# Kernel tuning notes

Measured on AMD Instinct MI355X. Metric: run time of the kernel, lower is better.

The kernel has to match this reference:

```python
import jax, jax.numpy as jnp
import numpy as np
from jax import lax

N_TRACES = 128
TRACE_LEN = 32          # uniform trace length -> seq_len
INPUT_DIM = 64
HIDDEN_DIM = 128
BATCH = N_TRACES * TRACE_LEN  # 4096 events = batch_size


def setup_inputs() -> dict:
    key = jax.random.key(0)
    ks = jax.random.split(key, 12)
    s = 1.0 / np.sqrt(HIDDEN_DIM)
    u = lambda k, shape: jax.random.uniform(k, shape, jnp.float32, -s, s)
    return {
        "input": jax.random.normal(ks[0], (BATCH, INPUT_DIM), jnp.float32),
        # layer 0 LSTM params (gate order i,f,g,o as in torch)
        "W_ih0": u(ks[1], (4 * HIDDEN_DIM, INPUT_DIM)),
        "W_hh0": u(ks[2], (4 * HIDDEN_DIM, HIDDEN_DIM)),
        "b_ih0": u(ks[3], (4 * HIDDEN_DIM,)),
        "b_hh0": u(ks[4], (4 * HIDDEN_DIM,)),
        # layer 1 LSTM params
        "W_ih1": u(ks[5], (4 * HIDDEN_DIM, HIDDEN_DIM)),
        "W_hh1": u(ks[6], (4 * HIDDEN_DIM, HIDDEN_DIM)),
        "b_ih1": u(ks[7], (4 * HIDDEN_DIM,)),
        "b_hh1": u(ks[8], (4 * HIDDEN_DIM,)),
        # final linear: hidden -> 1
        "W_lin": u(ks[9], (1, HIDDEN_DIM)),
        "b_lin": u(ks[10], (1,)),
    }


def _lstm_layer(xs, W_ih, W_hh, b_ih, b_hh):
    # xs: [T, B, D_in] time-major. Returns hidden stream [T, B, H].
    H = W_hh.shape[1]
    B = xs.shape[1]
    # precompute input projection for all timesteps
    x_proj = jnp.einsum('tbd,gd->tbg', xs, W_ih) + b_ih + b_hh  # [T,B,4H]

    def step(carry, xp):
        h, c = carry
        gates = xp + h @ W_hh.T                # [B,4H]
        i, f, g, o = jnp.split(gates, 4, axis=-1)
        i = jax.nn.sigmoid(i)
        f = jax.nn.sigmoid(f)
        g = jnp.tanh(g)
        o = jax.nn.sigmoid(o)
        c = f * c + i * g
        h = o * jnp.tanh(c)
        return (h, c), h

    h0 = jnp.zeros((B, H), xs.dtype)
    _, hs = lax.scan(step, (h0, h0), x_proj)
    return hs


def _forward(input, W_ih0, W_hh0, b_ih0, b_hh0, W_ih1, W_hh1, b_ih1, b_hh1, W_lin, b_lin):
    L, D = TRACE_LEN, INPUT_DIM
    # Prefix scatter: event k of a trace gets the padded prefix events[0..k].
    x_tr = input.reshape(N_TRACES, L, D)                       # [Ntr, L, D]
    causal = (jnp.arange(L)[None, :] <= jnp.arange(L)[:, None])  # [k, j] mask j<=k
    padded = x_tr[:, None, :, :] * causal[None, :, :, None].astype(input.dtype)  # [Ntr,L(k),L(j),D]
    padded = padded.reshape(BATCH, L, D)                       # batch-first padded sequences

    xs = jnp.transpose(padded, (1, 0, 2))                      # [L, B, D] time-major
    h1 = _lstm_layer(xs, W_ih0, W_hh0, b_ih0, b_hh0)           # [L, B, H]
    h2 = _lstm_layer(h1, W_ih1, W_hh1, b_ih1, b_hh1)           # [L, B, H]

    out = jnp.einsum('tbh,oh->tbo', h2, W_lin) + b_lin         # [L, B, 1]
    # last valid timestep gather: lengths[i]-1 = (i mod L)
    lens_m1 = jnp.tile(jnp.arange(L), N_TRACES)                # [B]
    y_pred = out[lens_m1, jnp.arange(BATCH), 0]                # [B]
    return y_pred


def reference(input, W_ih0, W_hh0, b_ih0, b_hh0, W_ih1, W_hh1, b_ih1, b_hh1, W_lin, b_lin):
    return _forward(input, W_ih0, W_hh0, b_ih0, b_hh0, W_ih1, W_hh1, b_ih1, b_hh1, W_lin, b_lin)
```

## Files before the change

kernel.cpp:

```cpp
#include <hip/hip_runtime.h>

#define N_TRACES 128
#define TLEN 32
#define IN_DIM 64
#define HID 128
#define G4 (4 * HID)
#define BATCH (N_TRACES * TLEN)


__device__ __forceinline__ float fast_sigmoid(float x) {
    return 1.0f / (1.0f + __expf(-x));
}
__device__ __forceinline__ float fast_tanh(float x) {
    return 1.0f - 2.0f / (__expf(2.0f * x) + 1.0f);
}
__device__ __forceinline__ float quad_reduce(float x) {
    x += __int_as_float(__builtin_amdgcn_update_dpp(
        0, __float_as_int(x), 0xB1 , 0xF, 0xF, true));
    x += __int_as_float(__builtin_amdgcn_update_dpp(
        0, __float_as_int(x), 0x4E , 0xF, 0xF, true));
    return x;
}

__device__ __forceinline__ void load_w(const float* __restrict__ W, int u, int s,
                                       float (&w)[4][32]) {
    #pragma unroll
    for (int i = 0; i < 4; ++i) {
        const float* wr = W + (size_t)(u + 128 * i) * HID + 32 * s;
        #pragma unroll
        for (int j = 0; j < 8; ++j) {
            float4 v = *(const float4*)(wr + 4 * j);
            w[i][4 * j + 0] = v.x; w[i][4 * j + 1] = v.y;
            w[i][4 * j + 2] = v.z; w[i][4 * j + 3] = v.w;
        }
    }
    #pragma unroll
    for (int i = 0; i < 4; ++i)
        #pragma unroll
        for (int j = 0; j < 32; ++j)
            asm volatile("" : "+v"(w[i][j]));
}

__device__ __forceinline__ void matvec_acc(const float (&w)[4][32],
                                           const float* hb, float (&acc)[4]) {
    #pragma unroll
    for (int j = 0; j < 8; ++j) {
        float4 v = *(const float4*)(hb + 4 * j);
        float hx[4] = {v.x, v.y, v.z, v.w};
        #pragma unroll
        for (int e = 0; e < 4; ++e) {
            #pragma unroll
            for (int i = 0; i < 4; ++i)
                acc[i] = fmaf(w[i][4 * j + e], hx[e], acc[i]);
        }
    }
}


template <int K>
__global__ __launch_bounds__(256) void gemm_bt(
    const float* __restrict__ A,
    const float* __restrict__ W,
    const float* __restrict__ b1,
    const float* __restrict__ b2,
    float* __restrict__ out,
    int Nld)
{
    constexpr int LD = 68;
    __shared__ float At[K][LD];
    __shared__ float Wt[K][LD];

    const int tid = threadIdx.x;
    const int m0 = blockIdx.x * 64;
    const int n0 = blockIdx.y * 64;

    const int rot = tid & 3;
    #pragma unroll
    for (int j = 0; j < K / 16; ++j) {
        const int e = 4 * (tid + 256 * j);
        const int row = e / K;
        const int k = e % K;
        float4 va = *(const float4*)(A + (size_t)(m0 + row) * K + k);
        float4 vw = *(const float4*)(W + (size_t)(n0 + row) * K + k);
        float fa[4] = {va.x, va.y, va.z, va.w};
        float fw[4] = {vw.x, vw.y, vw.z, vw.w};
        #pragma unroll
        for (int ii = 0; ii < 4; ++ii) {
            const int i = (ii + rot) & 3;
            At[k + i][row] = fa[i];
            Wt[k + i][row] = fw[i];
        }
    }
    __syncthreads();

    const int tx = tid & 15;
    const int ty = tid >> 4;
    float acc[4][4] = {};

    #pragma unroll 4
    for (int k = 0; k < K; ++k) {
        float4 a = *(const float4*)&At[k][ty * 4];
        float4 w = *(const float4*)&Wt[k][tx * 4];
        acc[0][0] = fmaf(a.x, w.x, acc[0][0]); acc[0][1] = fmaf(a.x, w.y, acc[0][1]);
        acc[0][2] = fmaf(a.x, w.z, acc[0][2]); acc[0][3] = fmaf(a.x, w.w, acc[0][3]);
        acc[1][0] = fmaf(a.y, w.x, acc[1][0]); acc[1][1] = fmaf(a.y, w.y, acc[1][1]);
        acc[1][2] = fmaf(a.y, w.z, acc[1][2]); acc[1][3] = fmaf(a.y, w.w, acc[1][3]);
        acc[2][0] = fmaf(a.z, w.x, acc[2][0]); acc[2][1] = fmaf(a.z, w.y, acc[2][1]);
        acc[2][2] = fmaf(a.z, w.z, acc[2][2]); acc[2][3] = fmaf(a.z, w.w, acc[2][3]);
        acc[3][0] = fmaf(a.w, w.x, acc[3][0]); acc[3][1] = fmaf(a.w, w.y, acc[3][1]);
        acc[3][2] = fmaf(a.w, w.z, acc[3][2]); acc[3][3] = fmaf(a.w, w.w, acc[3][3]);
    }

    float bb[4];
    #pragma unroll
    for (int j = 0; j < 4; ++j) {
        const int n = n0 + tx * 4 + j;
        bb[j] = b1[n] + b2[n];
    }
    #pragma unroll
    for (int i = 0; i < 4; ++i) {
        const int m = m0 + ty * 4 + i;
        float4 v;
        v.x = acc[i][0] + bb[0]; v.y = acc[i][1] + bb[1];
        v.z = acc[i][2] + bb[2]; v.w = acc[i][3] + bb[3];
        *(float4*)(out + (size_t)m * Nld + n0 + tx * 4) = v;
    }
}


__global__ __launch_bounds__(512) void fused_trace(
    const float* __restrict__ xproj0,
    const float* __restrict__ Whh0,
    const float* __restrict__ Wih1,
    const float* __restrict__ bih1,
    const float* __restrict__ bhh1,
    const float* __restrict__ Whh1,
    const float* __restrict__ Wlin,
    const float* __restrict__ blin,
    float* __restrict__ y)
{
    const int trace = blockIdx.x;
    const int tid = threadIdx.x;
    const int u = tid >> 2;
    const int s = tid & 3;
    const int pu = u + 4 * (u >> 5);

    __shared__ float hs[TLEN][140];
    __shared__ float xp[TLEN * G4];

    float w[4][32];

    const float* xpb = xproj0 + (size_t)trace * TLEN * G4;
    #pragma unroll
    for (int j = 0; j < 8; ++j) {
        const int f4 = j * 512 + tid;
        float4 v = *(const float4*)(xpb + 4 * f4);
        *(float4*)(&xp[4 * f4]) = v;
    }
    load_w(Whh0, u, s, w);
    __syncthreads();

    float c = 0.0f;
    #pragma unroll 1
    for (int t = 0; t < TLEN; ++t) {
        float xg[4];
        #pragma unroll
        for (int i = 0; i < 4; ++i) xg[i] = xp[t * G4 + 128 * i + u];

        float acc[4] = {0.f, 0.f, 0.f, 0.f};
        if (t > 0) matvec_acc(w, &hs[t - 1][36 * s], acc);
        #pragma unroll
        for (int i = 0; i < 4; ++i) acc[i] = quad_reduce(acc[i]);

        if (s == 0) {
            const float iv = fast_sigmoid(acc[0] + xg[0]);
            const float fv = fast_sigmoid(acc[1] + xg[1]);
            const float gv = fast_tanh(acc[2] + xg[2]);
            const float ov = fast_sigmoid(acc[3] + xg[3]);
            c = fv * c + iv * gv;
            hs[t][pu] = ov * fast_tanh(c);
        }
        __syncthreads();
    }

    load_w(Wih1, u, s, w);
    float bi[4] = {0.f, 0.f, 0.f, 0.f};
    if (s == 0) {
        #pragma unroll
        for (int i = 0; i < 4; ++i) bi[i] = bih1[u + 128 * i] + bhh1[u + 128 * i];
    }
    #pragma unroll 1
    for (int t = 0; t < TLEN; ++t) {
        float acc[4] = {0.f, 0.f, 0.f, 0.f};
        matvec_acc(w, &hs[t][36 * s], acc);
        #pragma unroll
        for (int i = 0; i < 4; ++i) acc[i] = quad_reduce(acc[i]);
        if (s == 0) {
            #pragma unroll
            for (int i = 0; i < 4; ++i) xp[t * G4 + 128 * i + u] = acc[i] + bi[i];
        }
    }
    __syncthreads();

    load_w(Whh1, u, s, w);
    c = 0.0f;
    #pragma unroll 1
    for (int t = 0; t < TLEN; ++t) {
        float xg[4];
        #pragma unroll
        for (int i = 0; i < 4; ++i) xg[i] = xp[t * G4 + 128 * i + u];

        float acc[4] = {0.f, 0.f, 0.f, 0.f};
        if (t > 0) matvec_acc(w, &hs[t - 1][36 * s], acc);
        #pragma unroll
        for (int i = 0; i < 4; ++i) acc[i] = quad_reduce(acc[i]);

        if (s == 0) {
            const float iv = fast_sigmoid(acc[0] + xg[0]);
            const float fv = fast_sigmoid(acc[1] + xg[1]);
            const float gv = fast_tanh(acc[2] + xg[2]);
            const float ov = fast_sigmoid(acc[3] + xg[3]);
            c = fv * c + iv * gv;
            hs[t][pu] = ov * fast_tanh(c);
        }
        __syncthreads();
    }

    if (tid < 128) {
        const int tq = tid >> 2;
        const int sq = tid & 3;
        float wl[32];
        #pragma unroll
        for (int j = 0; j < 8; ++j) {
            float4 v = *(const float4*)(Wlin + 32 * sq + 4 * j);
            wl[4 * j + 0] = v.x; wl[4 * j + 1] = v.y;
            wl[4 * j + 2] = v.z; wl[4 * j + 3] = v.w;
        }
        const float* hb = &hs[tq][36 * sq];
        float a = 0.f;
        #pragma unroll
        for (int j = 0; j < 8; ++j) {
            float4 v = *(const float4*)(hb + 4 * j);
            a = fmaf(v.x, wl[4 * j + 0], a);
            a = fmaf(v.y, wl[4 * j + 1], a);
            a = fmaf(v.z, wl[4 * j + 2], a);
            a = fmaf(v.w, wl[4 * j + 3], a);
        }
        a = quad_reduce(a);
        if (sq == 0) y[trace * TLEN + tq] = a + blin[0];
    }
}


extern "C" void kernel_launch(void* const* d_in, const int* in_sizes, int n_in,
                              void* d_out, int out_size, void* d_ws, size_t ws_size,
                              hipStream_t stream) {
    const float* input = (const float*)d_in[0];
    const float* W_ih0 = (const float*)d_in[1];
    const float* W_hh0 = (const float*)d_in[2];
    const float* b_ih0 = (const float*)d_in[3];
    const float* b_hh0 = (const float*)d_in[4];
    const float* W_ih1 = (const float*)d_in[5];
    const float* W_hh1 = (const float*)d_in[6];
    const float* b_ih1 = (const float*)d_in[7];
    const float* b_hh1 = (const float*)d_in[8];
    const float* W_lin = (const float*)d_in[9];
    const float* b_lin = (const float*)d_in[10];
    float* out = (float*)d_out;

    float* xproj0 = (float*)d_ws;

    dim3 ggrid(BATCH / 64, G4 / 64);

    gemm_bt<IN_DIM><<<ggrid, 256, 0, stream>>>(input, W_ih0, b_ih0, b_hh0, xproj0, G4);
    fused_trace<<<N_TRACES, 512, 0, stream>>>(xproj0, W_hh0, W_ih1, b_ih1, b_hh1,
                                              W_hh1, W_lin, b_lin, out);
}
```

Measured before the change: 167.9 us.

## Batch 16 traces per workgroup and run LSTM recurrences on bf16x3 MFMA

```diff
diff --git a/kernel.cpp b/kernel.cpp
--- a/kernel.cpp
+++ b/kernel.cpp
@@ -4,9 +4,13 @@
 #define TLEN 32
 #define IN_DIM 64
 #define HID 128
-#define G4 (4 * HID)
-#define BATCH (N_TRACES * TLEN)
-
+#define G4 512
+#define BATCH 4096
+#define WGT 16
+#define NWG 8
+
+typedef __attribute__((ext_vector_type(8))) short bf16x8;
+typedef __attribute__((ext_vector_type(4))) float f32x4;
 
 __device__ __forceinline__ float fast_sigmoid(float x) {
     return 1.0f / (1.0f + __expf(-x));
@@ -14,46 +18,12 @@
 __device__ __forceinline__ float fast_tanh(float x) {
     return 1.0f - 2.0f / (__expf(2.0f * x) + 1.0f);
 }
-__device__ __forceinline__ float quad_reduce(float x) {
-    x += __int_as_float(__builtin_amdgcn_update_dpp(
-        0, __float_as_int(x), 0xB1 , 0xF, 0xF, true));
-    x += __int_as_float(__builtin_amdgcn_update_dpp(
-        0, __float_as_int(x), 0x4E , 0xF, 0xF, true));
-    return x;
-}
-
-__device__ __forceinline__ void load_w(const float* __restrict__ W, int u, int s,
-                                       float (&w)[4][32]) {
-    #pragma unroll
-    for (int i = 0; i < 4; ++i) {
-        const float* wr = W + (size_t)(u + 128 * i) * HID + 32 * s;
-        #pragma unroll
-        for (int j = 0; j < 8; ++j) {
-            float4 v = *(const float4*)(wr + 4 * j);
-            w[i][4 * j + 0] = v.x; w[i][4 * j + 1] = v.y;
-            w[i][4 * j + 2] = v.z; w[i][4 * j + 3] = v.w;
-        }
-    }
-    #pragma unroll
-    for (int i = 0; i < 4; ++i)
-        #pragma unroll
-        for (int j = 0; j < 32; ++j)
-            asm volatile("" : "+v"(w[i][j]));
-}
-
-__device__ __forceinline__ void matvec_acc(const float (&w)[4][32],
-                                           const float* hb, float (&acc)[4]) {
-    #pragma unroll
-    for (int j = 0; j < 8; ++j) {
-        float4 v = *(const float4*)(hb + 4 * j);
-        float hx[4] = {v.x, v.y, v.z, v.w};
-        #pragma unroll
-        for (int e = 0; e < 4; ++e) {
-            #pragma unroll
-            for (int i = 0; i < 4; ++i)
-                acc[i] = fmaf(w[i][4 * j + e], hx[e], acc[i]);
-        }
-    }
+__device__ __forceinline__ short f2bf(float f) {
+    unsigned u = __float_as_uint(f);
+    return (short)((u + 0x7FFFu + ((u >> 16) & 1u)) >> 16);
+}
+__device__ __forceinline__ float bf2f(short h) {
+    return __uint_as_float(((unsigned)(unsigned short)h) << 16);
 }
 
 
@@ -128,7 +98,7 @@
 }
 
 
-__global__ __launch_bounds__(512) void fused_trace(
+__global__ __launch_bounds__(512, 2) void lstm_mfma(
     const float* __restrict__ xproj0,
     const float* __restrict__ Whh0,
     const float* __restrict__ Wih1,
@@ -137,117 +107,212 @@
     const float* __restrict__ Whh1,
     const float* __restrict__ Wlin,
     const float* __restrict__ blin,
+    float* __restrict__ wsh1g,
+    float* __restrict__ wsxp1g,
     float* __restrict__ y)
 {
-    const int trace = blockIdx.x;
+    const int wg  = blockIdx.x;
     const int tid = threadIdx.x;
-    const int u = tid >> 2;
-    const int s = tid & 3;
-    const int pu = u + 4 * (u >> 5);
-
-    __shared__ float hs[TLEN][140];
-    __shared__ float xp[TLEN * G4];
-
-    float w[4][32];
-
-    const float* xpb = xproj0 + (size_t)trace * TLEN * G4;
-    #pragma unroll
-    for (int j = 0; j < 8; ++j) {
-        const int f4 = j * 512 + tid;
-        float4 v = *(const float4*)(xpb + 4 * f4);
-        *(float4*)(&xp[4 * f4]) = v;
-    }
-    load_w(Whh0, u, s, w);
-    __syncthreads();
-
-    float c = 0.0f;
+    const int l   = tid & 63;
+    const int q   = tid >> 6;
+    const int ln  = l & 15;
+    const int qd  = l >> 4;
+    const int u0  = q * 16 + qd * 4;
+
+    __shared__ float hx[2][128 * 17];
+    __shared__ float ypart[2][8][16];
+
+    float* __restrict__ wsh1  = wsh1g  + (size_t)wg * (TLEN * 4 * 2 * 256);
+    float* __restrict__ wsxp1 = wsxp1g + (size_t)wg * (TLEN * 8 * 4 * 256);
+
+    bf16x8 Ah[4][4], Al[4][4];
+    bf16x8 Bh[4], Bl[4];
+    f32x4 xg[4];
+    float cc[4];
+
+    auto load_A = [&](const float* W) {
+        #pragma unroll
+        for (int i = 0; i < 4; ++i) {
+            const float* rp = W + (size_t)((q + 8 * i) * 16 + ln) * HID + qd * 8;
+            #pragma unroll
+            for (int kt = 0; kt < 4; ++kt) {
+                float4 a = *(const float4*)(rp + kt * 32);
+                float4 b = *(const float4*)(rp + kt * 32 + 4);
+                float f[8] = {a.x, a.y, a.z, a.w, b.x, b.y, b.z, b.w};
+                bf16x8 hi, lo;
+                #pragma unroll
+                for (int j = 0; j < 8; ++j) {
+                    short hb = f2bf(f[j]);
+                    hi[j] = hb;
+                    lo[j] = f2bf(f[j] - bf2f(hb));
+                }
+                Ah[i][kt] = hi; Al[i][kt] = lo;
+            }
+        }
+    };
+    auto zero_B = [&]() {
+        #pragma unroll
+        for (int kt = 0; kt < 4; ++kt)
+            #pragma unroll
+            for (int j = 0; j < 8; ++j) { Bh[kt][j] = 0; Bl[kt][j] = 0; }
+    };
+    auto build_B = [&](const float* hbuf) {
+        #pragma unroll
+        for (int kt = 0; kt < 4; ++kt) {
+            bf16x8 hi, lo;
+            #pragma unroll
+            for (int j = 0; j < 8; ++j) {
+                float f = hbuf[(kt * 32 + qd * 8 + j) * 17 + ln];
+                short hb = f2bf(f);
+                hi[j] = hb; lo[j] = f2bf(f - bf2f(hb));
+            }
+            Bh[kt] = hi; Bl[kt] = lo;
+        }
+    };
+    auto mfma_all = [&](f32x4 (&acc)[4]) {
+        #pragma unroll
+        for (int kt = 0; kt < 4; ++kt) {
+            #pragma unroll
+            for (int i = 0; i < 4; ++i) {
+                acc[i] = __builtin_amdgcn_mfma_f32_16x16x32_bf16(Ah[i][kt], Bh[kt], acc[i], 0, 0, 0);
+                acc[i] = __builtin_amdgcn_mfma_f32_16x16x32_bf16(Ah[i][kt], Bl[kt], acc[i], 0, 0, 0);
+                acc[i] = __builtin_amdgcn_mfma_f32_16x16x32_bf16(Al[i][kt], Bh[kt], acc[i], 0, 0, 0);
+            }
+        }
+    };
+
+    load_A(Whh0);
+    zero_B();
+    #pragma unroll
+    for (int r = 0; r < 4; ++r) cc[r] = 0.f;
+    const float* xpbase = xproj0 + (size_t)(wg * WGT + ln) * TLEN * G4;
+    #pragma unroll
+    for (int i = 0; i < 4; ++i)
+        xg[i] = *(const f32x4*)(xpbase + i * 128 + u0);
+
     #pragma unroll 1
     for (int t = 0; t < TLEN; ++t) {
-        float xg[4];
-        #pragma unroll
-        for (int i = 0; i < 4; ++i) xg[i] = xp[t * G4 + 128 * i + u];
-
-        float acc[4] = {0.f, 0.f, 0.f, 0.f};
-        if (t > 0) matvec_acc(w, &hs[t - 1][36 * s], acc);
-        #pragma unroll
-        for (int i = 0; i < 4; ++i) acc[i] = quad_reduce(acc[i]);
-
-        if (s == 0) {
-            const float iv = fast_sigmoid(acc[0] + xg[0]);
-            const float fv = fast_sigmoid(acc[1] + xg[1]);
-            const float gv = fast_tanh(acc[2] + xg[2]);
-            const float ov = fast_sigmoid(acc[3] + xg[3]);
-            c = fv * c + iv * gv;
-            hs[t][pu] = ov * fast_tanh(c);
-        }
+        f32x4 acc[4] = {f32x4{0,0,0,0}, f32x4{0,0,0,0}, f32x4{0,0,0,0}, f32x4{0,0,0,0}};
+        mfma_all(acc);
+        float h[4];
+        #pragma unroll
+        for (int r = 0; r < 4; ++r) {
+            float iv = fast_sigmoid(acc[0][r] + xg[0][r]);
+            float fv = fast_sigmoid(acc[1][r] + xg[1][r]);
+            float gv = fast_tanh  (acc[2][r] + xg[2][r]);
+            float ov = fast_sigmoid(acc[3][r] + xg[3][r]);
+            cc[r] = fv * cc[r] + iv * gv;
+            h[r]  = ov * fast_tanh(cc[r]);
+        }
+        float* hb = hx[t & 1];
+        #pragma unroll
+        for (int r = 0; r < 4; ++r) hb[(u0 + r) * 17 + ln] = h[r];
         __syncthreads();
-    }
-
-    load_w(Wih1, u, s, w);
-    float bi[4] = {0.f, 0.f, 0.f, 0.f};
-    if (s == 0) {
-        #pragma unroll
-        for (int i = 0; i < 4; ++i) bi[i] = bih1[u + 128 * i] + bhh1[u + 128 * i];
-    }
+        if (t + 1 < TLEN) {
+            #pragma unroll
+            for (int i = 0; i < 4; ++i)
+                xg[i] = *(const f32x4*)(xpbase + (size_t)(t + 1) * G4 + i * 128 + u0);
+        }
+        build_B(hb);
+        if (q == 0) {
+            #pragma unroll
+            for (int kt = 0; kt < 4; ++kt) {
+                *(float4*)(wsh1 + ((size_t)(t * 4 + kt) * 2 + 0) * 256 + l * 4) = *(float4*)&Bh[kt];
+                *(float4*)(wsh1 + ((size_t)(t * 4 + kt) * 2 + 1) * 256 + l * 4) = *(float4*)&Bl[kt];
+            }
+        }
+    }
+    __syncthreads();
+
+    load_A(Wih1);
+    f32x4 bias[4];
+    #pragma unroll
+    for (int i = 0; i < 4; ++i) {
+        f32x4 b1 = *(const f32x4*)(bih1 + (q + 8 * i) * 16 + qd * 4);
+        f32x4 b2 = *(const f32x4*)(bhh1 + (q + 8 * i) * 16 + qd * 4);
+        bias[i] = b1 + b2;
+    }
+    float4 bufA[8], bufB[8];
+    auto loadBraw = [&](int t, float4 (&buf)[8]) {
+        #pragma unroll
+        for (int kt = 0; kt < 4; ++kt) {
+            buf[kt * 2 + 0] = *(const float4*)(wsh1 + ((size_t)(t * 4 + kt) * 2 + 0) * 256 + l * 4);
+            buf[kt * 2 + 1] = *(const float4*)(wsh1 + ((size_t)(t * 4 + kt) * 2 + 1) * 256 + l * 4);
+        }
+    };
+    auto computeC = [&](int t, float4 (&buf)[8]) {
+        f32x4 acc[4] = {f32x4{0,0,0,0}, f32x4{0,0,0,0}, f32x4{0,0,0,0}, f32x4{0,0,0,0}};
+        #pragma unroll
+        for (int kt = 0; kt < 4; ++kt) {
+            bf16x8 bh = *(bf16x8*)&buf[kt * 2 + 0];
+            bf16x8 bl = *(bf16x8*)&buf[kt * 2 + 1];
+            #pragma unroll
+            for (int i = 0; i < 4; ++i) {
+                acc[i] = __builtin_amdgcn_mfma_f32_16x16x32_bf16(Ah[i][kt], bh, acc[i], 0, 0, 0);
+                acc[i] = __builtin_amdgcn_mfma_f32_16x16x32_bf16(Ah[i][kt], bl, acc[i], 0, 0, 0);
+                acc[i] = __builtin_amdgcn_mfma_f32_16x16x32_bf16(Al[i][kt], bh, acc[i], 0, 0, 0);
+            }
+        }
+        #pragma unroll
+        for (int i = 0; i < 4; ++i) {
+            f32x4 o = acc[i] + bias[i];
+            *(f32x4*)(wsxp1 + ((size_t)(t * 8 + q) * 4 + i) * 256 + l * 4) = o;
+        }
+    };
+    loadBraw(0, bufA);
+    #pragma unroll 1
+    for (int tt = 0; tt < TLEN / 2; ++tt) {
+        loadBraw(tt * 2 + 1, bufB);
+        computeC(tt * 2, bufA);
+        if (tt * 2 + 2 < TLEN) loadBraw(tt * 2 + 2, bufA);
+        computeC(tt * 2 + 1, bufB);
+    }
+    __syncthreads();
+
+    load_A(Whh1);
+    f32x4 wl = *(const f32x4*)(Wlin + u0);
+    float bl = blin[0];
+    zero_B();
+    #pragma unroll
+    for (int r = 0; r < 4; ++r) cc[r] = 0.f;
+    #pragma unroll
+    for (int i = 0; i < 4; ++i)
+        xg[i] = *(const f32x4*)(wsxp1 + ((size_t)(0 * 8 + q) * 4 + i) * 256 + l * 4);
+
     #pragma unroll 1
     for (int t = 0; t < TLEN; ++t) {
-        float acc[4] = {0.f, 0.f, 0.f, 0.f};
-        matvec_acc(w, &hs[t][36 * s], acc);
-        #pragma unroll
-        for (int i = 0; i < 4; ++i) acc[i] = quad_reduce(acc[i]);
-        if (s == 0) {
-            #pragma unroll
-            for (int i = 0; i < 4; ++i) xp[t * G4 + 128 * i + u] = acc[i] + bi[i];
-        }
-    }
-    __syncthreads();
-
-    load_w(Whh1, u, s, w);
-    c = 0.0f;
-    #pragma unroll 1
-    for (int t = 0; t < TLEN; ++t) {
-        float xg[4];
-        #pragma unroll
-        for (int i = 0; i < 4; ++i) xg[i] = xp[t * G4 + 128 * i + u];
-
-        float acc[4] = {0.f, 0.f, 0.f, 0.f};
-        if (t > 0) matvec_acc(w, &hs[t - 1][36 * s], acc);
-        #pragma unroll
-        for (int i = 0; i < 4; ++i) acc[i] = quad_reduce(acc[i]);
-
-        if (s == 0) {
-            const float iv = fast_sigmoid(acc[0] + xg[0]);
-            const float fv = fast_sigmoid(acc[1] + xg[1]);
-            const float gv = fast_tanh(acc[2] + xg[2]);
-            const float ov = fast_sigmoid(acc[3] + xg[3]);
-            c = fv * c + iv * gv;
-            hs[t][pu] = ov * fast_tanh(c);
-        }
+        f32x4 acc[4] = {f32x4{0,0,0,0}, f32x4{0,0,0,0}, f32x4{0,0,0,0}, f32x4{0,0,0,0}};
+        mfma_all(acc);
+        float h[4];
+        #pragma unroll
+        for (int r = 0; r < 4; ++r) {
+            float iv = fast_sigmoid(acc[0][r] + xg[0][r]);
+            float fv = fast_sigmoid(acc[1][r] + xg[1][r]);
+            float gv = fast_tanh  (acc[2][r] + xg[2][r]);
+            float ov = fast_sigmoid(acc[3][r] + xg[3][r]);
+            cc[r] = fv * cc[r] + iv * gv;
+            h[r]  = ov * fast_tanh(cc[r]);
+        }
+        float p = wl[0] * h[0] + wl[1] * h[1] + wl[2] * h[2] + wl[3] * h[3];
+        p += __shfl_xor(p, 16);
+        p += __shfl_xor(p, 32);
+        if (l < 16) ypart[t & 1][q][l] = p;
+        float* hb = hx[t & 1];
+        #pragma unroll
+        for (int r = 0; r < 4; ++r) hb[(u0 + r) * 17 + ln] = h[r];
         __syncthreads();
-    }
-
-    if (tid < 128) {
-        const int tq = tid >> 2;
-        const int sq = tid & 3;
-        float wl[32];
-        #pragma unroll
-        for (int j = 0; j < 8; ++j) {
-            float4 v = *(const float4*)(Wlin + 32 * sq + 4 * j);
-            wl[4 * j + 0] = v.x; wl[4 * j + 1] = v.y;
-            wl[4 * j + 2] = v.z; wl[4 * j + 3] = v.w;
-        }
-        const float* hb = &hs[tq][36 * sq];
-        float a = 0.f;
-        #pragma unroll
-        for (int j = 0; j < 8; ++j) {
-            float4 v = *(const float4*)(hb + 4 * j);
-            a = fmaf(v.x, wl[4 * j + 0], a);
-            a = fmaf(v.y, wl[4 * j + 1], a);
-            a = fmaf(v.z, wl[4 * j + 2], a);
-            a = fmaf(v.w, wl[4 * j + 3], a);
-        }
-        a = quad_reduce(a);
-        if (sq == 0) y[trace * TLEN + tq] = a + blin[0];
+        if (t + 1 < TLEN) {
+            #pragma unroll
+            for (int i = 0; i < 4; ++i)
+                xg[i] = *(const f32x4*)(wsxp1 + ((size_t)((t + 1) * 8 + q) * 4 + i) * 256 + l * 4);
+        }
+        build_B(hb);
+        if (q == 0 && l < 16) {
+            float s = bl;
+            #pragma unroll
+            for (int ww = 0; ww < 8; ++ww) s += ypart[t & 1][ww][l];
+            y[(size_t)(wg * WGT + l) * TLEN + t] = s;
+        }
     }
 }
 
@@ -269,10 +334,11 @@
     float* out = (float*)d_out;
 
     float* xproj0 = (float*)d_ws;
+    float* wsh1   = xproj0 + (size_t)BATCH * G4;
+    float* wsxp1  = wsh1 + (size_t)NWG * TLEN * 4 * 2 * 256;
 
     dim3 ggrid(BATCH / 64, G4 / 64);
-
     gemm_bt<IN_DIM><<<ggrid, 256, 0, stream>>>(input, W_ih0, b_ih0, b_hh0, xproj0, G4);
-    fused_trace<<<N_TRACES, 512, 0, stream>>>(xproj0, W_hh0, W_ih1, b_ih1, b_hh1,
-                                              W_hh1, W_lin, b_lin, out);
-}
+    lstm_mfma<<<NWG, 512, 0, stream>>>(xproj0, W_hh0, W_ih1, b_ih1, b_hh1,
+                                       W_hh1, W_lin, b_lin, wsh1, wsxp1, out);
+}
```

Measured after the change: 358.4 us. 113% more time.
